# Optimization experiments

Measured on AMD Instinct MI355X. Metric: run time of the kernel, lower is better.

The kernel has to match this reference:

```python
import jax, jax.numpy as jnp
import numpy as np

N_DELTA, N_THETA, N_GAMMA = 64, 128, 512
N_TOTAL = N_DELTA + N_THETA + N_GAMMA  # 704
N_CLASSES = 1000
N_STEPS = 5
DT = 0.01
COUPLING = 2.0      # coupling_strength
PAC_DT = 0.3        # delta->theta phase-amplitude coupling depth
PAC_TG = 0.3        # theta->gamma phase-amplitude coupling depth
SPARSITY = 0.1      # PhaseToRateConverter sparsity (fraction of active units)
SHARP = 10.0        # softness of the 'soft' sparsification gate
TWO_PI = 2.0 * np.pi
B = 65536


def setup_inputs() -> dict:
    key = jax.random.key(0)
    k1, k2, k3, k4 = jax.random.split(key, 4)
    x = jax.random.normal(k1, (B, N_TOTAL), dtype=jnp.float32)
    # per-sample random initial phases in [0,1), scaled to [0,2pi) inside reference
    phase0 = jax.random.uniform(k2, (B, N_TOTAL), dtype=jnp.float32)
    W = jax.random.normal(k3, (N_CLASSES, N_TOTAL), dtype=jnp.float32) * 0.02
    b = jax.random.normal(k4, (N_CLASSES,), dtype=jnp.float32) * 0.02
    return {"x": x, "phase0": phase0, "W": W, "b": b}


def _kuramoto(phi):
    # mean-field within-band Kuramoto coupling: K * mean_j sin(phi_j - phi_i)
    S = jnp.mean(jnp.sin(phi), axis=-1, keepdims=True)
    C = jnp.mean(jnp.cos(phi), axis=-1, keepdims=True)
    return COUPLING * (S * jnp.cos(phi) - C * jnp.sin(phi))


def _mean_phase(phi):
    # circular mean phase of a band, shape (B,1)
    return jnp.arctan2(jnp.mean(jnp.sin(phi), axis=-1, keepdims=True),
                       jnp.mean(jnp.cos(phi), axis=-1, keepdims=True))


def _forward(x, phase0, W, b):
    freqs = jnp.concatenate([
        jnp.linspace(1.0, 4.0, N_DELTA),    # delta band Hz
        jnp.linspace(4.0, 8.0, N_THETA),    # theta band Hz
        jnp.linspace(30.0, 80.0, N_GAMMA),  # gamma band Hz
    ]).astype(x.dtype)
    phi = phase0 * TWO_PI                       # (B, N_TOTAL)
    amp = 1.0 + jnp.abs(x) * 0.01               # amplitude seeded by |x|*0.01 on unit base
    d = slice(0, N_DELTA)
    t = slice(N_DELTA, N_DELTA + N_THETA)
    g = slice(N_DELTA + N_THETA, N_TOTAL)

    def step(carry, _):
        phi, amp = carry
        dphi = TWO_PI * freqs + jnp.concatenate(
            [_kuramoto(phi[:, d]), _kuramoto(phi[:, t]), _kuramoto(phi[:, g])], axis=-1)
        psi_d = _mean_phase(phi[:, d])
        psi_t = _mean_phase(phi[:, t])
        # PAC: theta amplitude driven by delta phase, gamma amplitude by theta phase
        damp = jnp.concatenate([
            jnp.zeros_like(amp[:, d]),
            PAC_DT * amp[:, t] * jnp.cos(psi_d),
            PAC_TG * amp[:, g] * jnp.cos(psi_t),
        ], axis=-1)
        phi_new = jnp.mod(phi + DT * dphi, TWO_PI)
        amp_new = amp + DT * damp
        return (phi_new, amp_new), None

    (phi, amp), _ = jax.lax.scan(step, (phi, amp), None, length=N_STEPS)

    # PhaseToRateConverter, mode='soft': raw rate then soft top-(sparsity) gate
    raw = amp * 0.5 * (1.0 + jnp.cos(phi))                              # (B, N_TOTAL)
    thr = jnp.quantile(raw, 1.0 - SPARSITY, axis=-1, keepdims=True)    # per-sample threshold
    rate = raw * jax.nn.sigmoid((raw - thr) * SHARP)
    return rate @ W.T + b                                               # (B, N_CLASSES)


def reference(x, phase0, W, b):
    return _forward(x, phase0, W, b)
```

## Files before the change

### kernel.cpp

```cpp
#include <hip/hip_runtime.h>

#define NB 65536
#define NTOT 704
#define NCLS 1000
#define NPAD 1024
#define KDIM 704

typedef __attribute__((ext_vector_type(8))) short bf16x8;
typedef __attribute__((ext_vector_type(4))) float f32x4;
typedef __attribute__((ext_vector_type(2))) float f32x2;

#define WB_ELEMS (NPAD * KDIM)
#define LUT_DC_OFF (2u * (WB_ELEMS + 46137344u))
#define LUT_DS_OFF (LUT_DC_OFF + NTOT * 4u)

__device__ __forceinline__ f32x2 sp(float x) { return (f32x2){x, x}; }

template <int CTRL>
__device__ __forceinline__ float dpp_shuf(float v) {
  return __int_as_float(__builtin_amdgcn_update_dpp(0, __float_as_int(v), CTRL, 0xF, 0xF, true));
}
__device__ __forceinline__ float swz16(float v) {
  return __int_as_float(__builtin_amdgcn_ds_swizzle(__float_as_int(v), 0x401F));
}
__device__ __forceinline__ float wsum_f(float v) {
  v += dpp_shuf<0xB1>(v);
  v += dpp_shuf<0x4E>(v);
  v += dpp_shuf<0x141>(v);
  v += dpp_shuf<0x140>(v);
  v += swz16(v);
  v += __shfl_xor(v, 32, 64);
  return v;
}
__device__ __forceinline__ float wmax_f(float v) {
  v = fmaxf(v, dpp_shuf<0xB1>(v));
  v = fmaxf(v, dpp_shuf<0x4E>(v));
  v = fmaxf(v, dpp_shuf<0x141>(v));
  v = fmaxf(v, dpp_shuf<0x140>(v));
  v = fmaxf(v, swz16(v));
  v = fmaxf(v, __shfl_xor(v, 32, 64));
  return v;
}
__device__ __forceinline__ float wmin_f(float v) {
  v = fminf(v, dpp_shuf<0xB1>(v));
  v = fminf(v, dpp_shuf<0x4E>(v));
  v = fminf(v, dpp_shuf<0x141>(v));
  v = fminf(v, dpp_shuf<0x140>(v));
  v = fminf(v, swz16(v));
  v = fminf(v, __shfl_xor(v, 32, 64));
  return v;
}

__device__ __forceinline__ unsigned short f2bf(float v) {
  unsigned u = __float_as_uint(v);
  u = (u + 0x7FFFu + ((u >> 16) & 1u)) >> 16;
  return (unsigned short)u;
}

__global__ __launch_bounds__(256) void convw_kernel(const float* __restrict__ W,
                                                    unsigned short* __restrict__ Wb,
                                                    float* __restrict__ dcL,
                                                    float* __restrict__ dsL) {
  int i = blockIdx.x * 256 + threadIdx.x;
  if (i < NTOT) {
    float f;
    if (i < 64)       f = 1.0f + 3.0f * (float)i * (1.0f / 63.0f);
    else if (i < 192) f = 4.0f + 4.0f * (float)(i - 64) * (1.0f / 127.0f);
    else              f = 30.0f + 50.0f * (float)(i - 192) * (1.0f / 511.0f);
    const float rev = 0.01f * f;
    dcL[i] = __builtin_amdgcn_cosf(rev);
    dsL[i] = __builtin_amdgcn_sinf(rev);
  }
  if (i >= NPAD * KDIM) return;
  int n = i / KDIM;
  float v = (n < NCLS) ? W[i] : 0.0f;
  Wb[i] = f2bf(v);
}

__global__ __launch_bounds__(256) void sim_kernel(const float* __restrict__ x,
                                                  const float* __restrict__ p0,
                                                  const float* __restrict__ dcL,
                                                  const float* __restrict__ dsL,
                                                  unsigned short* __restrict__ rateb) {
  const int wave = threadIdx.x >> 6;
  const int lane = threadIdx.x & 63;
  const int sample = blockIdx.x * 4 + wave;
  const size_t base = (size_t)sample * NTOT;

  float sD, cD, ampD, dcD, dsD;
  f32x2 sPp[5], cPp[5], dc2[5], ds2[5], amp2[5];
  {
    const float p = p0[base + lane];
    sD = __builtin_amdgcn_sinf(p);
    cD = __builtin_amdgcn_cosf(p);
    ampD = fmaf(fabsf(x[base + lane]), 0.01f, 1.0f);
    dcD = dcL[lane]; dsD = dsL[lane];
  }
#pragma unroll
  for (int pr = 0; pr < 5; ++pr) {
    const int i0 = (1 + 2 * pr) * 64 + lane;
    const int i1 = i0 + 64;
    const float pa = p0[base + i0], pb = p0[base + i1];
    sPp[pr] = (f32x2){__builtin_amdgcn_sinf(pa), __builtin_amdgcn_sinf(pb)};
    cPp[pr] = (f32x2){__builtin_amdgcn_cosf(pa), __builtin_amdgcn_cosf(pb)};
    amp2[pr] = (f32x2){fmaf(fabsf(x[base + i0]), 0.01f, 1.0f),
                       fmaf(fabsf(x[base + i1]), 0.01f, 1.0f)};
    dc2[pr] = (f32x2){dcL[i0], dcL[i1]};
    ds2[pr] = (f32x2){dsL[i0], dsL[i1]};
  }

  float prodT = 1.0f, prodG = 1.0f;

#pragma unroll
  for (int st = 0; st < 5; ++st) {
    const float Sd = wsum_f(sD);
    const float Cd = wsum_f(cD);
    const float St = wsum_f(sPp[0].x + sPp[0].y);
    const float Ct = wsum_f(cPp[0].x + cPp[0].y);
    const f32x2 gs = (sPp[1] + sPp[2]) + (sPp[3] + sPp[4]);
    const f32x2 gc = (cPp[1] + cPp[2]) + (cPp[3] + cPp[4]);
    const float Sg = wsum_f(gs.x + gs.y);
    const float Cg = wsum_f(gc.x + gc.y);
    const float cpd = Cd * __builtin_amdgcn_rsqf(fmaf(Sd, Sd, Cd * Cd));
    const float cpt = Ct * __builtin_amdgcn_rsqf(fmaf(St, St, Ct * Ct));
    prodT *= fmaf(0.003f, cpd, 1.0f);
    prodG *= fmaf(0.003f, cpt, 1.0f);
    const float sdm = Sd * (0.02f / 64.0f),  cdm = Cd * (0.02f / 64.0f);
    const float stm = St * (0.02f / 128.0f), ctm = Ct * (0.02f / 128.0f);
    const float sgm = Sg * (0.02f / 512.0f), cgm = Cg * (0.02f / 512.0f);
    {
      const float eps = fmaf(-cdm, sD, sdm * cD);
      const float cd_ = fmaf(-dsD, eps, dcD);
      const float sd_ = fmaf(dcD, eps, dsD);
      const float sn = fmaf(cD, sd_, sD * cd_);
      const float cn = fmaf(-sD, sd_, cD * cd_);
      sD = sn; cD = cn;
    }
#pragma unroll
    for (int pr = 0; pr < 5; ++pr) {
      const f32x2 Sm = sp(pr == 0 ? stm : sgm);
      const f32x2 Cm = sp(pr == 0 ? ctm : cgm);
      const f32x2 s2 = sPp[pr], c2 = cPp[pr];
      const f32x2 eps = Sm * c2 - Cm * s2;
      const f32x2 cosd = dc2[pr] - ds2[pr] * eps;
      const f32x2 sind = ds2[pr] + dc2[pr] * eps;
      sPp[pr] = s2 * cosd + c2 * sind;
      cPp[pr] = c2 * cosd - s2 * sind;
    }
  }

  float raw[11];
  unsigned kk[11];
  {
    const float h = 0.5f * ampD;
    raw[0] = fmaf(h, cD, h);
  }
  const float hT = 0.5f * prodT, hG = 0.5f * prodG;
#pragma unroll
  for (int pr = 0; pr < 5; ++pr) {
    const f32x2 h2 = amp2[pr] * sp(pr == 0 ? hT : hG);
    const f32x2 r2 = h2 * cPp[pr] + h2;
    raw[1 + 2 * pr] = r2.x;
    raw[2 + 2 * pr] = r2.y;
  }
#pragma unroll
  for (int e = 0; e < 11; ++e) kk[e] = (unsigned)(raw[e] * 8192.0f);

  unsigned pre = 0;
#pragma unroll
  for (int bit = 13; bit >= 0; --bit) {
    const unsigned u = pre | ((1u << bit) - 1u);
    int cnt = 0;
#pragma unroll
    for (int e = 0; e < 11; ++e) cnt += (int)__popcll(__ballot(kk[e] <= u));
    if (cnt < 633) pre |= (1u << bit);
  }

  int clt = 0, ceq = 0;
#pragma unroll
  for (int e = 0; e < 11; ++e) {
    clt += (int)__popcll(__ballot(kk[e] < pre));
    ceq += (int)__popcll(__ballot(kk[e] == pre));
  }

  const float qv = 0.9f * 703.0f;
  float thr;
  if (clt + ceq >= 634) {
    thr = ((float)pre + 0.5f) * (1.0f / 8192.0f);
  } else {
    float mx = -1.0f, mn = 3.0e38f;
#pragma unroll
    for (int e = 0; e < 11; ++e) {
      mx = fmaxf(mx, (kk[e] == pre) ? raw[e] : -1.0f);
      mn = fminf(mn, (kk[e] > pre) ? raw[e] : 3.0e38f);
    }
    const float S632 = wmax_f(mx);
    const float S633 = wmin_f(mn);
    thr = S632 * (633.0f - qv) + S633 * (qv - 632.0f);
  }

#pragma unroll
  for (int e = 0; e < 11; ++e) {
    const float r = raw[e];
    const float t = __expf((thr - r) * 10.0f);
    const float sg = __builtin_amdgcn_rcpf(1.0f + t);
    rateb[base + e * 64 + lane] = f2bf(r * sg);
  }
}

#define BK3 64
#define NK3 (KDIM / BK3)

#define FENCE __builtin_amdgcn_sched_barrier(0)
#define BAR   do { FENCE; __builtin_amdgcn_s_barrier(); FENCE; } while (0)
#define WVM8  do { asm volatile("s_waitcnt vmcnt(8)"); FENCE; } while (0)
#define WVM0  do { asm volatile("s_waitcnt vmcnt(0)"); FENCE; } while (0)
#define WLG0  do { asm volatile("s_waitcnt lgkmcnt(0)"); FENCE; } while (0)

__device__ __forceinline__ void gload16(const unsigned short* g, unsigned short* l) {
  __builtin_amdgcn_global_load_lds((const __attribute__((address_space(1))) void*)g,
                                   (__attribute__((address_space(3))) void*)l,
                                   16, 0, 0);
}

__global__ __launch_bounds__(512, 2) void gemm_kernel(const unsigned short* __restrict__ A,
                                                      const unsigned short* __restrict__ Bw,
                                                      const float* __restrict__ bias,
                                                      float* __restrict__ C) {
  __shared__ __align__(16) unsigned short lsA[4 * 8192];
  __shared__ __align__(16) unsigned short lsB[4 * 8192];
  const int tid  = threadIdx.x;
  const int wave = tid >> 6;
  const int lane = tid & 63;

  const int bid = blockIdx.x;
  const int swz = (bid & 7) * 128 + (bid >> 3);
  const int bm = swz >> 2;
  const int bn = swz & 3;

  const int wr = wave >> 2;
  const int wc = wave & 3;

  f32x4 acc[8][4];
#pragma unroll
  for (int i = 0; i < 8; ++i)
#pragma unroll
    for (int j = 0; j < 4; ++j) acc[i][j] = (f32x4){0.f, 0.f, 0.f, 0.f};

  const int srow = tid >> 3;
  const int sc16 = ((tid & 7) ^ (srow & 7)) * 8;
  const unsigned short* Ab = A  + (size_t)(bm * 256) * KDIM;
  const unsigned short* Bb = Bw + (size_t)(bn * 256) * KDIM;

#define SHALF(dst, srcb, rb, k0)                                                      \
  gload16((srcb) + (size_t)((rb) + srow) * KDIM + (k0) + sc16, (dst) + tid * 8);      \
  gload16((srcb) + (size_t)((rb) + 64 + srow) * KDIM + (k0) + sc16, (dst) + 4096 + tid * 8);

  SHALF(lsA + 0 * 8192, Ab, 0, 0)
  SHALF(lsA + 1 * 8192, Ab, 128, 0)
  SHALF(lsB + 0 * 8192, Bb, 0, 0)
  SHALF(lsB + 1 * 8192, Bb, 128, 0)
  SHALF(lsA + 2 * 8192, Ab, 0, BK3)
  SHALF(lsA + 3 * 8192, Ab, 128, BK3)
  SHALF(lsB + 2 * 8192, Bb, 0, BK3)
  SHALF(lsB + 3 * 8192, Bb, 128, BK3)

  const int l15 = lane & 15;
  const int kq  = lane >> 4;

  bf16x8 af[4][2];
  bf16x8 bg[4][2];

#pragma unroll 1
  for (int t = 0; t < NK3; ++t) {
    const int d = t & 1;
    const int k2 = (t + 2) * BK3;
    const bool stg = (t + 2) < NK3;
    const unsigned short* hA = lsA + (d * 2 + wr) * 8192;
    const unsigned short* hB = lsB + (d * 2 + (wc >> 1)) * 8192;
    const int rB0 = (wc & 1) * 64;

    if (t == NK3 - 1) { WVM0; } else { WVM8; }
    BAR;
#pragma unroll
    for (int m = 0; m < 4; ++m) {
      const int lr = m * 16 + l15;
      af[m][0] = *(const bf16x8*)&hA[lr * 64 + ((kq ^ (lr & 7)) * 8)];
      af[m][1] = *(const bf16x8*)&hA[lr * 64 + (((kq + 4) ^ (lr & 7)) * 8)];
    }
#pragma unroll
    for (int n = 0; n < 2; ++n) {
      const int lr = rB0 + n * 16 + l15;
      bg[n][0] = *(const bf16x8*)&hB[lr * 64 + ((kq ^ (lr & 7)) * 8)];
      bg[n][1] = *(const bf16x8*)&hB[lr * 64 + (((kq + 4) ^ (lr & 7)) * 8)];
    }
    WLG0;
    __builtin_amdgcn_s_setprio(1);
#pragma unroll
    for (int m = 0; m < 4; ++m)
#pragma unroll
      for (int n = 0; n < 2; ++n) {
        acc[m][n] = __builtin_amdgcn_mfma_f32_16x16x32_bf16(af[m][0], bg[n][0], acc[m][n], 0, 0, 0);
        acc[m][n] = __builtin_amdgcn_mfma_f32_16x16x32_bf16(af[m][1], bg[n][1], acc[m][n], 0, 0, 0);
      }
    __builtin_amdgcn_s_setprio(0);
    FENCE;

#pragma unroll
    for (int n = 2; n < 4; ++n) {
      const int lr = rB0 + n * 16 + l15;
      bg[n][0] = *(const bf16x8*)&hB[lr * 64 + ((kq ^ (lr & 7)) * 8)];
      bg[n][1] = *(const bf16x8*)&hB[lr * 64 + (((kq + 4) ^ (lr & 7)) * 8)];
    }
    WLG0;
    BAR;
    if (stg) {
      SHALF(lsB + (d * 2 + 0) * 8192, Bb, 0, k2)
      SHALF(lsB + (d * 2 + 1) * 8192, Bb, 128, k2)
    }
    FENCE;
    __builtin_amdgcn_s_setprio(1);
#pragma unroll
    for (int m = 0; m < 4; ++m)
#pragma unroll
      for (int n = 2; n < 4; ++n) {
        acc[m][n] = __builtin_amdgcn_mfma_f32_16x16x32_bf16(af[m][0], bg[n][0], acc[m][n], 0, 0, 0);
        acc[m][n] = __builtin_amdgcn_mfma_f32_16x16x32_bf16(af[m][1], bg[n][1], acc[m][n], 0, 0, 0);
      }
    __builtin_amdgcn_s_setprio(0);
    FENCE;

#pragma unroll
    for (int m = 0; m < 4; ++m) {
      const int lr = (m + 4) * 16 + l15;
      af[m][0] = *(const bf16x8*)&hA[lr * 64 + ((kq ^ (lr & 7)) * 8)];
      af[m][1] = *(const bf16x8*)&hA[lr * 64 + (((kq + 4) ^ (lr & 7)) * 8)];
    }
    WLG0;
    BAR;
    if (stg) {
      SHALF(lsA + (d * 2 + 0) * 8192, Ab, 0, k2)
      SHALF(lsA + (d * 2 + 1) * 8192, Ab, 128, k2)
    }
    FENCE;
    __builtin_amdgcn_s_setprio(1);
#pragma unroll
    for (int m = 0; m < 4; ++m)
#pragma unroll
      for (int n = 0; n < 2; ++n) {
        acc[m + 4][n] = __builtin_amdgcn_mfma_f32_16x16x32_bf16(af[m][0], bg[n][0], acc[m + 4][n], 0, 0, 0);
        acc[m + 4][n] = __builtin_amdgcn_mfma_f32_16x16x32_bf16(af[m][1], bg[n][1], acc[m + 4][n], 0, 0, 0);
      }
    __builtin_amdgcn_s_setprio(0);
    FENCE;

    __builtin_amdgcn_s_setprio(1);
#pragma unroll
    for (int m = 0; m < 4; ++m)
#pragma unroll
      for (int n = 2; n < 4; ++n) {
        acc[m + 4][n] = __builtin_amdgcn_mfma_f32_16x16x32_bf16(af[m][0], bg[n][0], acc[m + 4][n], 0, 0, 0);
        acc[m + 4][n] = __builtin_amdgcn_mfma_f32_16x16x32_bf16(af[m][1], bg[n][1], acc[m + 4][n], 0, 0, 0);
      }
    __builtin_amdgcn_s_setprio(0);
    FENCE;
  }

  const int crow0 = bm * 256 + wr * 128;
  const int ccol0 = bn * 256 + wc * 64;
  const int rql = (lane >> 4) * 4;
  const int cl  = lane & 15;
#pragma unroll
  for (int n = 0; n < 4; ++n) {
    const int col = ccol0 + n * 16 + cl;
    if (col < NCLS) {
      const float bb = bias[col];
#pragma unroll
      for (int m = 0; m < 8; ++m) {
#pragma unroll
        for (int r = 0; r < 4; ++r) {
          const int row = crow0 + m * 16 + rql + r;
          C[(size_t)row * NCLS + col] = acc[m][n][r] + bb;
        }
      }
    }
  }
}

extern "C" void kernel_launch(void* const* d_in, const int* in_sizes, int n_in,
                              void* d_out, int out_size, void* d_ws, size_t ws_size,
                              hipStream_t stream) {
  const float* x    = (const float*)d_in[0];
  const float* p0   = (const float*)d_in[1];
  const float* W    = (const float*)d_in[2];
  const float* bias = (const float*)d_in[3];
  float* out = (float*)d_out;

  unsigned short* Wb    = (unsigned short*)d_ws;
  unsigned short* rateb = (unsigned short*)d_ws + WB_ELEMS;
  float* dcL = (float*)((char*)d_ws + LUT_DC_OFF);
  float* dsL = (float*)((char*)d_ws + LUT_DS_OFF);

  convw_kernel<<<dim3((NPAD * KDIM + 255) / 256), dim3(256), 0, stream>>>(W, Wb, dcL, dsL);
  sim_kernel<<<dim3(NB / 4), dim3(256), 0, stream>>>(x, p0, dcL, dsL, rateb);
  gemm_kernel<<<dim3((NB / 256) * (NPAD / 256)), dim3(512), 0, stream>>>(rateb, Wb, bias, out);
}
```

Measured before the change: 295.9 us.

## Restructure GEMM LDS pipeline to prefetch one stage ahead with ping-pong barriers

Changes the GEMM main loop from a two-tiles-ahead prefetch with partial vmcnt waits to a one-tile-ahead ping-pong scheme. Loads of the next K tile are issued in pieces between the MFMA phases, with a barrier around each phase and a full vmcnt wait at the end of every iteration. The goal is to spread global-to-LDS traffic across the compute phases and to make buffer reuse safe with simpler counting. In exchange it adds more barriers per iteration, and the shallower prefetch depth may leave load latency exposed.

```diff
diff --git a/kernel.cpp b/kernel.cpp
--- a/kernel.cpp
+++ b/kernel.cpp
@@ -213,7 +213,6 @@
 
 #define FENCE __builtin_amdgcn_sched_barrier(0)
 #define BAR   do { FENCE; __builtin_amdgcn_s_barrier(); FENCE; } while (0)
-#define WVM8  do { asm volatile("s_waitcnt vmcnt(8)"); FENCE; } while (0)
 #define WVM0  do { asm volatile("s_waitcnt vmcnt(0)"); FENCE; } while (0)
 #define WLG0  do { asm volatile("s_waitcnt lgkmcnt(0)"); FENCE; } while (0)
 
@@ -260,10 +259,8 @@
   SHALF(lsA + 1 * 8192, Ab, 128, 0)
   SHALF(lsB + 0 * 8192, Bb, 0, 0)
   SHALF(lsB + 1 * 8192, Bb, 128, 0)
-  SHALF(lsA + 2 * 8192, Ab, 0, BK3)
-  SHALF(lsA + 3 * 8192, Ab, 128, BK3)
-  SHALF(lsB + 2 * 8192, Bb, 0, BK3)
-  SHALF(lsB + 3 * 8192, Bb, 128, BK3)
+  WVM0;
+  BAR;
 
   const int l15 = lane & 15;
   const int kq  = lane >> 4;
@@ -273,15 +270,13 @@
 
 #pragma unroll 1
   for (int t = 0; t < NK3; ++t) {
-    const int d = t & 1;
-    const int k2 = (t + 2) * BK3;
-    const bool stg = (t + 2) < NK3;
-    const unsigned short* hA = lsA + (d * 2 + wr) * 8192;
-    const unsigned short* hB = lsB + (d * 2 + (wc >> 1)) * 8192;
+    const int c = t & 1, nc = c ^ 1;
+    const int k1 = (t + 1) * BK3;
+    const bool stg = (t + 1) < NK3;
+    const unsigned short* hA = lsA + (c * 2 + wr) * 8192;
+    const unsigned short* hB = lsB + (c * 2 + (wc >> 1)) * 8192;
     const int rB0 = (wc & 1) * 64;
 
-    if (t == NK3 - 1) { WVM0; } else { WVM8; }
-    BAR;
 #pragma unroll
     for (int m = 0; m < 4; ++m) {
       const int lr = m * 16 + l15;
@@ -294,6 +289,8 @@
       bg[n][0] = *(const bf16x8*)&hB[lr * 64 + ((kq ^ (lr & 7)) * 8)];
       bg[n][1] = *(const bf16x8*)&hB[lr * 64 + (((kq + 4) ^ (lr & 7)) * 8)];
     }
+    if (stg) { SHALF(lsA + (nc * 2 + 0) * 8192, Ab, 0, k1) }
+    BAR;
     WLG0;
     __builtin_amdgcn_s_setprio(1);
 #pragma unroll
@@ -304,7 +301,7 @@
         acc[m][n] = __builtin_amdgcn_mfma_f32_16x16x32_bf16(af[m][1], bg[n][1], acc[m][n], 0, 0, 0);
       }
     __builtin_amdgcn_s_setprio(0);
-    FENCE;
+    BAR;
 
 #pragma unroll
     for (int n = 2; n < 4; ++n) {
@@ -312,13 +309,9 @@
       bg[n][0] = *(const bf16x8*)&hB[lr * 64 + ((kq ^ (lr & 7)) * 8)];
       bg[n][1] = *(const bf16x8*)&hB[lr * 64 + (((kq + 4) ^ (lr & 7)) * 8)];
     }
+    if (stg) { SHALF(lsA + (nc * 2 + 1) * 8192, Ab, 128, k1) }
+    BAR;
     WLG0;
-    BAR;
-    if (stg) {
-      SHALF(lsB + (d * 2 + 0) * 8192, Bb, 0, k2)
-      SHALF(lsB + (d * 2 + 1) * 8192, Bb, 128, k2)
-    }
-    FENCE;
     __builtin_amdgcn_s_setprio(1);
 #pragma unroll
     for (int m = 0; m < 4; ++m)
@@ -328,7 +321,7 @@
         acc[m][n] = __builtin_amdgcn_mfma_f32_16x16x32_bf16(af[m][1], bg[n][1], acc[m][n], 0, 0, 0);
       }
     __builtin_amdgcn_s_setprio(0);
-    FENCE;
+    BAR;
 
 #pragma unroll
     for (int m = 0; m < 4; ++m) {
@@ -336,13 +329,12 @@
       af[m][0] = *(const bf16x8*)&hA[lr * 64 + ((kq ^ (lr & 7)) * 8)];
       af[m][1] = *(const bf16x8*)&hA[lr * 64 + (((kq + 4) ^ (lr & 7)) * 8)];
     }
+    if (stg) {
+      SHALF(lsB + (nc * 2 + 0) * 8192, Bb, 0, k1)
+      SHALF(lsB + (nc * 2 + 1) * 8192, Bb, 128, k1)
+    }
+    BAR;
     WLG0;
-    BAR;
-    if (stg) {
-      SHALF(lsA + (d * 2 + 0) * 8192, Ab, 0, k2)
-      SHALF(lsA + (d * 2 + 1) * 8192, Ab, 128, k2)
-    }
-    FENCE;
     __builtin_amdgcn_s_setprio(1);
 #pragma unroll
     for (int m = 0; m < 4; ++m)
@@ -352,7 +344,7 @@
         acc[m + 4][n] = __builtin_amdgcn_mfma_f32_16x16x32_bf16(af[m][1], bg[n][1], acc[m + 4][n], 0, 0, 0);
       }
     __builtin_amdgcn_s_setprio(0);
-    FENCE;
+    BAR;
 
     __builtin_amdgcn_s_setprio(1);
 #pragma unroll
@@ -364,6 +356,8 @@
       }
     __builtin_amdgcn_s_setprio(0);
     FENCE;
+    if (stg) { WVM0; }
+    BAR;
   }
 
   const int crow0 = bm * 256 + wr * 128;
```

Measured after the change: 300.3 us. About the same (+1.5%).
